# Kernel tuning notes

Measured on AMD Instinct MI355X. Metric: run time of the kernel, lower is better.

## Reference

```python
import jax, jax.numpy as jnp
import numpy as np

B, S, D = 4, 4096, 1024
DC = 1024  # d_chunk (defaults to d_model)
NUM_CLASSES = 4


def setup_inputs() -> dict:
    key = jax.random.key(0)
    ks = jax.random.split(key, 8)
    init = lambda k, shape: (jax.random.normal(k, shape, jnp.float32) * 0.02)
    return {
        "h": jax.random.normal(ks[0], (B, S, D), jnp.float32),
        "pseudo_labels": jax.random.randint(ks[1], (B, S), 0, NUM_CLASSES, jnp.int32),
        "Wl": init(ks[2], (D, NUM_CLASSES)), "bl": jnp.zeros((NUM_CLASSES,), jnp.float32),
        "Wq": init(ks[3], (D, DC)), "bq": jnp.zeros((DC,), jnp.float32),
        "Wk": init(ks[4], (D, DC)), "bk": jnp.zeros((DC,), jnp.float32),
        "Wv": init(ks[5], (D, D)), "bv": jnp.zeros((D,), jnp.float32),
        "Wo": init(ks[6], (D, D)), "bo": jnp.zeros((D,), jnp.float32),
    }


def _chunk_starts(labels):
    """BIOS chunking: label 0=B starts a chunk extended by following 1=I's;
    labels 1 (orphan I), 2=O, 3=S are singleton chunks. Returns bool [B,S]
    marking chunk starts. Parallel replacement for the torch while-loop."""
    def step(ext, lab):  # ext[b]: previous token can be extended by an I
        cont = (lab == 1) & ext          # this token continues prev chunk
        new_ext = (lab == 0) | cont      # B, or a continuing I, is extendable
        return new_ext, ~cont            # non-continuing token starts a chunk
    init = jnp.zeros(labels.shape[0], dtype=bool)
    _, starts_t = jax.lax.scan(step, init, labels.T)  # scan over seq axis
    return starts_t.T  # [B, S]


def reference(h, pseudo_labels, Wl, bl, Wq, bq, Wk, bk, Wv, bv, Wo, bo):
    b, s, d = h.shape
    dc = Wq.shape[1]

    logits = h @ Wl + bl                                  # [B,S,4]
    logp = jax.nn.log_softmax(logits, axis=-1)
    loss = -jnp.mean(jnp.take_along_axis(logp, pseudo_labels[..., None], axis=-1))

    pred = jnp.argmax(logits, axis=-1).astype(jnp.int32)  # [B,S]
    starts = _chunk_starts(pred)
    seg = jnp.cumsum(starts.astype(jnp.int32), axis=1) - 1  # segment id per token

    # Segment-mean pooling, padded to S possible chunks per batch element.
    seg_sum = jax.vmap(lambda x, ids: jax.ops.segment_sum(x, ids, num_segments=s))(h, seg)
    counts = jax.vmap(lambda ids: jax.ops.segment_sum(jnp.ones((s,), h.dtype), ids, num_segments=s))(seg)
    chunk_emb = seg_sum / jnp.maximum(counts, 1.0)[..., None]  # [B,S,D]
    valid = counts > 0                                         # [B,S]

    q = h @ Wq + bq              # [B,S,DC]
    k = chunk_emb @ Wk + bk      # [B,C,DC]
    v = chunk_emb @ Wv + bv      # [B,C,D]
    scale = jnp.asarray(1.0 / np.sqrt(dc), h.dtype)
    scores = jnp.einsum('bsd,bcd->bsc', q, k) * scale
    scores = jnp.where(valid[:, None, :], scores, jnp.asarray(-1e30, h.dtype))
    attn = jax.nn.softmax(scores, axis=-1)
    attended = jnp.einsum('bsc,bcd->bsd', attn, v)
    ch_out = attended @ Wo + bo
    return ch_out, loss
```

## Files before the change

kernel.cpp:

```cpp
#include <hip/hip_runtime.h>

typedef unsigned short u16;
typedef __attribute__((ext_vector_type(8))) short short8;
typedef __attribute__((ext_vector_type(8))) unsigned short ushort8;
typedef __attribute__((ext_vector_type(4))) unsigned short ushort4v;
typedef __attribute__((ext_vector_type(4))) float f32x4;

#define NB 4
#define SS 4096
#define DD 1024

__device__ __forceinline__ u16 f2bf(float x) {
  unsigned u = __builtin_bit_cast(unsigned, x);
  u = (u + 0x7FFFu + ((u >> 16) & 1u)) >> 16;
  return (u16)u;
}
__device__ __forceinline__ float bf2f(u16 b) {
  unsigned u = ((unsigned)b) << 16;
  return __builtin_bit_cast(float, u);
}
__device__ __forceinline__ void gload16(const void* g, void* l) {
  __builtin_amdgcn_global_load_lds((const __attribute__((address_space(1))) void*)g,
                                   (__attribute__((address_space(3))) void*)l, 16, 0, 0);
}
__device__ __forceinline__ int xcd_swz(int bid, int nwg) {
  const int x = bid & 7, idx = bid >> 3;
  const int q = nwg >> 3, r = nwg & 7;
  return (x < r ? x * (q + 1) : r * (q + 1) + (x - r) * q) + idx;
}

__global__ __launch_bounds__(256) void k_logits(
    const float* __restrict__ h, const int* __restrict__ lab,
    const float* __restrict__ Wl, const float* __restrict__ bl,
    u16* __restrict__ h16, int* __restrict__ pred, float* __restrict__ lossPart)
{
  const int t = threadIdx.x, w = t >> 6, lane = t & 63;
  const int tok = blockIdx.x * 4 + w;
  const float4* h4p = (const float4*)(h + (size_t)tok * DD);
  const float4* wl4 = (const float4*)Wl;
  float p0 = 0.f, p1 = 0.f, p2 = 0.f, p3 = 0.f;
#pragma unroll
  for (int i = 0; i < 4; ++i) {
    const int d = i * 256 + lane * 4;
    float4 hv = h4p[i * 64 + lane];
    ushort4v hb;
    hb[0] = f2bf(hv.x); hb[1] = f2bf(hv.y); hb[2] = f2bf(hv.z); hb[3] = f2bf(hv.w);
    *(ushort4v*)(h16 + (size_t)tok * DD + d) = hb;
    float4 w0 = wl4[d], w1 = wl4[d + 1], w2 = wl4[d + 2], w3 = wl4[d + 3];
    p0 += hv.x * w0.x + hv.y * w1.x + hv.z * w2.x + hv.w * w3.x;
    p1 += hv.x * w0.y + hv.y * w1.y + hv.z * w2.y + hv.w * w3.y;
    p2 += hv.x * w0.z + hv.y * w1.z + hv.z * w2.z + hv.w * w3.z;
    p3 += hv.x * w0.w + hv.y * w1.w + hv.z * w2.w + hv.w * w3.w;
  }
#pragma unroll
  for (int m = 32; m; m >>= 1) {
    p0 += __shfl_xor(p0, m); p1 += __shfl_xor(p1, m);
    p2 += __shfl_xor(p2, m); p3 += __shfl_xor(p3, m);
  }
  __shared__ float ls[4];
  if (lane == 0) {
    float l[4] = {p0 + bl[0], p1 + bl[1], p2 + bl[2], p3 + bl[3]};
    int bi = 0; float bv = l[0];
#pragma unroll
    for (int c = 1; c < 4; ++c) if (l[c] > bv) { bv = l[c]; bi = c; }
    pred[tok] = bi;
    float se = 0.f;
#pragma unroll
    for (int c = 0; c < 4; ++c) se += expf(l[c] - bv);
    float lse = bv + logf(se);
    ls[w] = lse - l[lab[tok]];
  }
  __syncthreads();
  if (t == 0) lossPart[blockIdx.x] = ls[0] + ls[1] + ls[2] + ls[3];
}

__global__ __launch_bounds__(256) void k_wconv(
    const float* __restrict__ W0, const float* __restrict__ W1,
    const float* __restrict__ W2, const float* __restrict__ W3,
    u16* __restrict__ Wt)
{
  const int gid = blockIdx.x * 256 + threadIdx.x;
  const int mat = gid >> 20;
  const int rem = gid & ((1 << 20) - 1);
  const int n = rem >> 10, k = rem & 1023;
  const float* W = (mat == 0) ? W0 : (mat == 1) ? W1 : (mat == 2) ? W2 : W3;
  Wt[((size_t)mat << 20) + (size_t)n * 1024 + k] = f2bf(W[(size_t)k * 1024 + n]);
}

__global__ __launch_bounds__(256) void k_scan(
    const int* __restrict__ pred, int* __restrict__ cstart, int* __restrict__ ccnt)
{
  const int b = blockIdx.x, t = threadIdx.x;
  const int4* p4 = (const int4*)(pred + (size_t)b * SS);
  int labv[16];
#pragma unroll
  for (int i = 0; i < 4; ++i) {
    int4 v = p4[t * 4 + i];
    labv[i * 4 + 0] = v.x; labv[i * 4 + 1] = v.y;
    labv[i * 4 + 2] = v.z; labv[i * 4 + 3] = v.w;
  }
  int A = 0, Bc = 1;
#pragma unroll
  for (int e = 0; e < 16; ++e) {
    int a = (labv[e] == 0), bb = (labv[e] == 1);
    A = a | (bb & A);
    Bc = bb & Bc;
  }
  __shared__ int sA[256], sB[256], sC[256];
  sA[t] = A; sB[t] = Bc;
  __syncthreads();
  for (int off = 1; off < 256; off <<= 1) {
    int pa = 0, pb = 1;
    if (t >= off) { pa = sA[t - off]; pb = sB[t - off]; }
    __syncthreads();
    A = A | (Bc & pa); Bc = Bc & pb;
    sA[t] = A; sB[t] = Bc;
    __syncthreads();
  }
  const int extIn = (t == 0) ? 0 : sA[t - 1];
  int ext = extIn, nst = 0;
#pragma unroll
  for (int e = 0; e < 16; ++e) {
    int cont = (labv[e] == 1) & ext;
    nst += !cont;
    ext = (labv[e] == 0) | cont;
  }
  sC[t] = nst;
  __syncthreads();
  int tot = nst;
  for (int off = 1; off < 256; off <<= 1) {
    int pc = 0;
    if (t >= off) pc = sC[t - off];
    __syncthreads();
    tot += pc;
    sC[t] = tot;
    __syncthreads();
  }
  const int base = tot - nst;
  const int total = sC[255];
  if (t == 0) { ccnt[b] = total; cstart[b * (SS + 1) + total] = SS; }
  ext = extIn; int id = base;
#pragma unroll
  for (int e = 0; e < 16; ++e) {
    int cont = (labv[e] == 1) & ext;
    if (!cont) cstart[b * (SS + 1) + id++] = t * 16 + e;
    ext = (labv[e] == 0) | cont;
  }
}

__global__ __launch_bounds__(256) void k_pool(
    const float* __restrict__ h, const int* __restrict__ cstart,
    const int* __restrict__ ccnt, u16* __restrict__ cemb)
{
  const int t = threadIdx.x, w = t >> 6, lane = t & 63;
  const int gw = blockIdx.x * 4 + w;
  const int b = gw >> 12, c = gw & (SS - 1);
  u16* out = cemb + (size_t)gw * DD + lane * 16;
  if (c >= ccnt[b]) {
    ushort8 z = {0, 0, 0, 0, 0, 0, 0, 0};
    *(ushort8*)out = z; *(ushort8*)(out + 8) = z;
    return;
  }
  const int s0 = cstart[b * (SS + 1) + c], s1 = cstart[b * (SS + 1) + c + 1];
  float acc[16] = {};
  for (int s = s0; s < s1; ++s) {
    const float4* hp = (const float4*)(h + ((size_t)b * SS + s) * DD + lane * 16);
#pragma unroll
    for (int ii = 0; ii < 4; ++ii) {
      float4 v = hp[ii];
      acc[ii * 4 + 0] += v.x; acc[ii * 4 + 1] += v.y;
      acc[ii * 4 + 2] += v.z; acc[ii * 4 + 3] += v.w;
    }
  }
  const float inv = 1.f / (float)(s1 - s0);
  ushort8 o0, o1;
#pragma unroll
  for (int e = 0; e < 8; ++e) { o0[e] = f2bf(acc[e] * inv); o1[e] = f2bf(acc[8 + e] * inv); }
  *(ushort8*)out = o0; *(ushort8*)(out + 8) = o1;
}

template <int OUTF32>
__global__ __launch_bounds__(512, 2) void gemm256(
    const u16* __restrict__ A0, const u16* __restrict__ A1,
    const u16* __restrict__ A2, const u16* __restrict__ A3,
    const u16* __restrict__ Bt, long strideB,
    void* __restrict__ C0, void* __restrict__ C1,
    void* __restrict__ C2, void* __restrict__ C3,
    const float* __restrict__ bias, float scale, int M, int N, int K)
{
  __shared__ u16 sA[2][256 * 64], sB[2][256 * 64];
  const int t = threadIdx.x, lane = t & 63, w = t >> 6;
  const int wr = w >> 2, wc = w & 3;
  const int z = blockIdx.z;
  const u16* A = (z == 0) ? A0 : (z == 1) ? A1 : (z == 2) ? A2 : A3;
  void* Cp    = (z == 0) ? C0 : (z == 1) ? C1 : (z == 2) ? C2 : C3;
  const u16* B = Bt + (size_t)z * strideB;
  const int bid = blockIdx.y * gridDim.x + blockIdx.x;
  const int swz = xcd_swz(bid, gridDim.x * gridDim.y);
  const int m0 = (swz / gridDim.x) * 256, n0 = (swz % gridDim.x) * 256;

  f32x4 acc[8][4];
#pragma unroll
  for (int i = 0; i < 8; ++i)
#pragma unroll
    for (int j = 0; j < 4; ++j) acc[i][j] = (f32x4){0.f, 0.f, 0.f, 0.f};

  const int trow = t >> 3;
  const int schunk = ((t & 7) ^ (trow & 7)) * 8;
  const u16* Ag = A + (size_t)(m0 + trow) * K + schunk;
  const u16* Bg = B + (size_t)(n0 + trow) * K + schunk;
  u16* lA = &sA[0][0] + t * 8;
  u16* lB = &sB[0][0] + t * 8;
  auto stage = [&](int c, int kt) {
#pragma unroll
    for (int g = 0; g < 4; ++g)
      gload16(Ag + (size_t)(g * 64) * K + kt, lA + c * 16384 + g * 4096);
#pragma unroll
    for (int g = 0; g < 4; ++g)
      gload16(Bg + (size_t)(g * 64) * K + kt, lB + c * 16384 + g * 4096);
  };

  const int lrow = lane & 15, hi = lane >> 4, sx = lrow & 7;
  auto compute = [&](int c) {
    const u16* bA = &sA[c][0];
    const u16* bB = &sB[c][0];
#pragma unroll
    for (int ks = 0; ks < 2; ++ks) {
      const int co = ((ks * 4 + hi) ^ sx) * 8;
      short8 af[8], bf[4];
#pragma unroll
      for (int m = 0; m < 8; ++m)
        af[m] = *(const short8*)(bA + (wr * 128 + m * 16 + lrow) * 64 + co);
#pragma unroll
      for (int n = 0; n < 4; ++n)
        bf[n] = *(const short8*)(bB + (wc * 64 + n * 16 + lrow) * 64 + co);
#pragma unroll
      for (int m = 0; m < 8; ++m)
#pragma unroll
        for (int n = 0; n < 4; ++n)
          acc[m][n] = __builtin_amdgcn_mfma_f32_16x16x32_bf16(af[m], bf[n], acc[m][n], 0, 0, 0);
    }
  };

  const int NT = K >> 6;
  stage(0, 0);
  if (NT > 1) { stage(1, 64); asm volatile("s_waitcnt vmcnt(8)" ::: "memory"); }
  else        { asm volatile("s_waitcnt vmcnt(0)" ::: "memory"); }
  __builtin_amdgcn_s_barrier();
  asm volatile("" ::: "memory");
  for (int i = 0; i < NT; ++i) {
    const int cur = i & 1;
    compute(cur);
    asm volatile("" ::: "memory");
    if (i + 2 < NT) {
      __builtin_amdgcn_s_barrier();
      asm volatile("" ::: "memory");
      stage(cur, (i + 2) * 64);
    }
    if (i + 1 < NT) {
      if (i + 2 < NT) asm volatile("s_waitcnt vmcnt(8)" ::: "memory");
      else            asm volatile("s_waitcnt vmcnt(0)" ::: "memory");
      __builtin_amdgcn_s_barrier();
      asm volatile("" ::: "memory");
    }
  }

  const int colb = n0 + wc * 64 + (lane & 15);
  const int rowb = m0 + wr * 128 + (lane >> 4) * 4;
#pragma unroll
  for (int n = 0; n < 4; ++n) {
    const int col = colb + n * 16;
    const float bv = bias ? bias[col] : 0.f;
#pragma unroll
    for (int m = 0; m < 8; ++m) {
#pragma unroll
      for (int qx = 0; qx < 4; ++qx) {
        const float v = acc[m][n][qx] * scale + bv;
        const size_t idx = (size_t)(rowb + m * 16 + qx) * N + col;
        if (OUTF32) ((float*)Cp)[idx] = v;
        else        ((u16*)Cp)[idx]  = f2bf(v);
      }
    }
  }
}

__global__ __launch_bounds__(256) void k_softmax(
    u16* __restrict__ s0, u16* __restrict__ s1,
    u16* __restrict__ s2, u16* __restrict__ s3, const int* __restrict__ ccnt)
{
  const int t = threadIdx.x, lane = t & 63, w = t >> 6;
  const int row = blockIdx.x, b = blockIdx.y;
  u16* sc = (b == 0) ? s0 : (b == 1) ? s1 : (b == 2) ? s2 : s3;
  const int Cb = ccnt[b];
  u16* p = sc + (size_t)row * SS + t * 16;
  ushort8 v0 = *(ushort8*)p, v1 = *(ushort8*)(p + 8);
  float x[16];
#pragma unroll
  for (int e = 0; e < 8; ++e) { x[e] = bf2f(v0[e]); x[8 + e] = bf2f(v1[e]); }
  const int cb0 = t * 16;
  float m = -1e30f;
#pragma unroll
  for (int e = 0; e < 16; ++e) if (cb0 + e < Cb) m = fmaxf(m, x[e]);
#pragma unroll
  for (int off = 32; off; off >>= 1) m = fmaxf(m, __shfl_xor(m, off));
  __shared__ float red[4], red2[4];
  if (lane == 0) red[w] = m;
  __syncthreads();
  m = fmaxf(fmaxf(red[0], red[1]), fmaxf(red[2], red[3]));
  float ssum = 0.f;
#pragma unroll
  for (int e = 0; e < 16; ++e) {
    float ev = (cb0 + e < Cb) ? __expf(x[e] - m) : 0.f;
    x[e] = ev; ssum += ev;
  }
#pragma unroll
  for (int off = 32; off; off >>= 1) ssum += __shfl_xor(ssum, off);
  if (lane == 0) red2[w] = ssum;
  __syncthreads();
  ssum = red2[0] + red2[1] + red2[2] + red2[3];
  const float inv = 1.f / ssum;
#pragma unroll
  for (int e = 0; e < 8; ++e) { v0[e] = f2bf(x[e] * inv); v1[e] = f2bf(x[8 + e] * inv); }
  *(ushort8*)p = v0; *(ushort8*)(p + 8) = v1;
}

__global__ __launch_bounds__(256) void k_transpose(
    const u16* __restrict__ v, u16* __restrict__ vt)
{
  __shared__ u16 ts[64][80];
  const int t = threadIdx.x;
  const int d0 = blockIdx.x * 64, c0 = blockIdx.y * 64, b = blockIdx.z;
#pragma unroll
  for (int p = 0; p < 2; ++p) {
    const int idx = p * 256 + t, r = idx >> 3, cc = idx & 7;
    ushort8 val = *(const ushort8*)(v + ((size_t)b * SS + c0 + r) * DD + d0 + cc * 8);
    *(ushort8*)&ts[r][cc * 8] = val;
  }
  __syncthreads();
#pragma unroll
  for (int p = 0; p < 2; ++p) {
    const int idx = p * 256 + t, r = idx >> 3, cc = idx & 7;
    ushort8 o;
#pragma unroll
    for (int e = 0; e < 8; ++e) o[e] = ts[cc * 8 + e][r];
    *(ushort8*)(vt + ((size_t)b * DD + d0 + r) * SS + c0 + cc * 8) = o;
  }
}

__global__ __launch_bounds__(256) void k_lossfin(
    const float* __restrict__ part, float* __restrict__ out)
{
  const int t = threadIdx.x, lane = t & 63, w = t >> 6;
  float s = 0.f;
  for (int i = t; i < 4096; i += 256) s += part[i];
#pragma unroll
  for (int off = 32; off; off >>= 1) s += __shfl_xor(s, off);
  __shared__ float r[4];
  if (lane == 0) r[w] = s;
  __syncthreads();
  if (t == 0) out[0] = (r[0] + r[1] + r[2] + r[3]) * (1.f / (NB * SS));
}

extern "C" void kernel_launch(void* const* d_in, const int* in_sizes, int n_in,
                              void* d_out, int out_size, void* d_ws, size_t ws_size,
                              hipStream_t stream) {
  const float* h  = (const float*)d_in[0];
  const int* plab = (const int*)d_in[1];
  const float* Wl = (const float*)d_in[2];
  const float* bl = (const float*)d_in[3];
  const float* Wq = (const float*)d_in[4];
  const float* bq = (const float*)d_in[5];
  const float* Wk = (const float*)d_in[6];
  const float* bk = (const float*)d_in[7];
  const float* Wv = (const float*)d_in[8];
  const float* bv = (const float*)d_in[9];
  const float* Wo = (const float*)d_in[10];
  const float* bo = (const float*)d_in[11];
  float* out = (float*)d_out;

  char* ws = (char*)d_ws;
  const size_t SZ = (size_t)NB * SS * DD * 2;
  const size_t SD = (size_t)SS * DD;
  u16* h16      = (u16*)(ws + 0 * SZ);
  u16* cemb     = (u16*)(ws + 1 * SZ);
  u16* q        = (u16*)(ws + 2 * SZ);
  u16* kk       = (u16*)(ws + 3 * SZ);
  u16* vv       = (u16*)(ws + 4 * SZ);
  u16* vt       = (u16*)(ws + 5 * SZ);
  u16* Wt       = (u16*)(ws + 6 * SZ);
  char* ws2     = ws + 6 * SZ + (size_t)4 * 1024 * 1024 * 2;
  int* pred     = (int*)ws2;
  int* cstart   = (int*)(ws2 + 65536);
  int* ccnt     = (int*)(ws2 + 65536 + 4 * (SS + 1) * 4);
  float* lossPart = (float*)(ws2 + 65536 + 4 * (SS + 1) * 4 + 64);
  u16* s0 = (u16*)d_out;
  u16* s1 = (u16*)d_out + (size_t)SS * SS;
  u16* s2 = h16;
  u16* s3 = cemb;
  u16* att = vv;

  k_logits<<<dim3(NB * SS / 4), 256, 0, stream>>>(h, plab, Wl, bl, h16, pred, lossPart);
  k_wconv<<<dim3(4 * 1024 * 1024 / 256), 256, 0, stream>>>(Wq, Wk, Wv, Wo, Wt);
  k_scan<<<dim3(NB), 256, 0, stream>>>(pred, cstart, ccnt);
  k_pool<<<dim3(NB * SS / 4), 256, 0, stream>>>(h, cstart, ccnt, cemb);

  gemm256<0><<<dim3(DD / 256, NB * SS / 256, 1), 512, 0, stream>>>(
      h16, h16, h16, h16, Wt, 0, q, q, q, q, bq, 1.f, NB * SS, DD, DD);
  gemm256<0><<<dim3(DD / 256, NB * SS / 256, 1), 512, 0, stream>>>(
      cemb, cemb, cemb, cemb, Wt + (1 << 20), 0, kk, kk, kk, kk, bk, 1.f, NB * SS, DD, DD);
  gemm256<0><<<dim3(DD / 256, NB * SS / 256, 1), 512, 0, stream>>>(
      cemb, cemb, cemb, cemb, Wt + 2 * (1 << 20), 0, vv, vv, vv, vv, bv, 1.f, NB * SS, DD, DD);
  k_transpose<<<dim3(DD / 64, SS / 64, NB), 256, 0, stream>>>(vv, vt);

  const float scl = 1.f / 32.f;
  gemm256<0><<<dim3(SS / 256, SS / 256, NB), 512, 0, stream>>>(
      q, q + SD, q + 2 * SD, q + 3 * SD, kk, (long)SD,
      s0, s1, s2, s3, nullptr, scl, SS, SS, DD);
  k_softmax<<<dim3(SS, NB), 256, 0, stream>>>(s0, s1, s2, s3, ccnt);
  gemm256<0><<<dim3(DD / 256, SS / 256, NB), 512, 0, stream>>>(
      s0, s1, s2, s3, vt, (long)SD,
      att, att + SD, att + 2 * SD, att + 3 * SD, nullptr, 1.f, SS, DD, SS);
  gemm256<1><<<dim3(DD / 256, NB * SS / 256, 1), 512, 0, stream>>>(
      att, att, att, att, Wt + 3 * (1 << 20), 0, out, out, out, out, bo, 1.f, NB * SS, DD, DD);
  k_lossfin<<<dim3(1), 256, 0, stream>>>(lossPart, out + (size_t)NB * SS * DD);
}
```

Baseline: 640.1 us.

## Restructure GEMM main loop into four-phase interleaved load/MFMA schedule with LDS-staged epilogue

Rewrites the 256x256 bf16 GEMM main loop so each K-tile is split into four quadrant phases. Each phase issues part of the next tiles' global-to-LDS loads, then runs a block of MFMAs under raised wave priority, with barriers and sched_barriers fencing the stages. The bf16 output path now stages results through LDS and writes 16-byte coalesced rows instead of scattered 2-byte stores. The aim is better overlap of memory traffic with MFMA work and cheaper stores. The cost is many more barriers per iteration and a changed column mapping of warps to tiles.

```diff
diff --git a/kernel.cpp b/kernel.cpp
--- a/kernel.cpp
+++ b/kernel.cpp
@@ -9,6 +9,7 @@
 #define NB 4
 #define SS 4096
 #define DD 1024
+#define CFENCE asm volatile("" ::: "memory")
 
 __device__ __forceinline__ u16 f2bf(float x) {
   unsigned u = __builtin_bit_cast(unsigned, x);
@@ -188,7 +189,9 @@
     void* __restrict__ C2, void* __restrict__ C3,
     const float* __restrict__ bias, float scale, int M, int N, int K)
 {
-  __shared__ u16 sA[2][256 * 64], sB[2][256 * 64];
+  __shared__ u16 lds[65536];
+  u16* ldsA = lds;
+  u16* ldsB = lds + 32768;
   const int t = threadIdx.x, lane = t & 63, w = t >> 6;
   const int wr = w >> 2, wc = w & 3;
   const int z = blockIdx.z;
@@ -206,82 +209,144 @@
     for (int j = 0; j < 4; ++j) acc[i][j] = (f32x4){0.f, 0.f, 0.f, 0.f};
 
   const int trow = t >> 3;
-  const int schunk = ((t & 7) ^ (trow & 7)) * 8;
-  const u16* Ag = A + (size_t)(m0 + trow) * K + schunk;
-  const u16* Bg = B + (size_t)(n0 + trow) * K + schunk;
-  u16* lA = &sA[0][0] + t * 8;
-  u16* lB = &sB[0][0] + t * 8;
-  auto stage = [&](int c, int kt) {
-#pragma unroll
-    for (int g = 0; g < 4; ++g)
-      gload16(Ag + (size_t)(g * 64) * K + kt, lA + c * 16384 + g * 4096);
-#pragma unroll
-    for (int g = 0; g < 4; ++g)
-      gload16(Bg + (size_t)(g * 64) * K + kt, lB + c * 16384 + g * 4096);
-  };
-
-  const int lrow = lane & 15, hi = lane >> 4, sx = lrow & 7;
-  auto compute = [&](int c) {
-    const u16* bA = &sA[c][0];
-    const u16* bB = &sB[c][0];
-#pragma unroll
-    for (int ks = 0; ks < 2; ++ks) {
-      const int co = ((ks * 4 + hi) ^ sx) * 8;
-      short8 af[8], bf[4];
+  const u16* Ag = A + (size_t)(m0 + trow) * K + ((t & 7) ^ (trow & 7)) * 8;
+  const u16* Bg = B + (size_t)(n0 + trow) * K + ((t & 7) ^ (trow & 7)) * 8;
+  u16* dA = ldsA + t * 8;
+  u16* dB = ldsB + t * 8;
+
+#define STG_A0(BUF, KT) { gload16(Ag + (size_t)(KT),            dA + (BUF) * 16384 + 0 * 4096); \
+                          gload16(Ag + (size_t)128 * K + (KT),  dA + (BUF) * 16384 + 2 * 4096); }
+#define STG_A1(BUF, KT) { gload16(Ag + (size_t)64 * K + (KT),   dA + (BUF) * 16384 + 1 * 4096); \
+                          gload16(Ag + (size_t)192 * K + (KT),  dA + (BUF) * 16384 + 3 * 4096); }
+#define STG_B0(BUF, KT) { gload16(Bg + (size_t)(KT),            dB + (BUF) * 16384 + 0 * 4096); \
+                          gload16(Bg + (size_t)64 * K + (KT),   dB + (BUF) * 16384 + 1 * 4096); }
+#define STG_B1(BUF, KT) { gload16(Bg + (size_t)128 * K + (KT),  dB + (BUF) * 16384 + 2 * 4096); \
+                          gload16(Bg + (size_t)192 * K + (KT),  dB + (BUF) * 16384 + 3 * 4096); }
+#define MFMA16(MH, NH, BF) \
+  { _Pragma("unroll") for (int ks = 0; ks < 2; ++ks) \
+    _Pragma("unroll") for (int mi = 0; mi < 4; ++mi) \
+      _Pragma("unroll") for (int ni = 0; ni < 2; ++ni) \
+        acc[(MH) * 4 + mi][(NH) * 2 + ni] = __builtin_amdgcn_mfma_f32_16x16x32_bf16( \
+            af[mi][ks], BF[ni][ks], acc[(MH) * 4 + mi][(NH) * 2 + ni], 0, 0, 0); }
+
+  const int lrow = lane & 15, hi = lane >> 4;
+  const int co0 = (hi ^ (lrow & 7)) * 8;
+  const int co1 = ((4 + hi) ^ (lrow & 7)) * 8;
+
+  const int NT = K >> 6;
+  STG_A0(0, 0); STG_B0(0, 0); STG_B1(0, 0); STG_A1(0, 0);
+  if (NT > 1) { STG_A0(1, 64); STG_B0(1, 64); STG_B1(1, 64); }
+  if (NT > 1) asm volatile("s_waitcnt vmcnt(6)" ::: "memory");
+  else        asm volatile("s_waitcnt vmcnt(0)" ::: "memory");
+  __builtin_amdgcn_s_barrier();
+  CFENCE;
+
+  for (int j = 0; j < NT; ++j) {
+    const int cur = j & 1;
+    const u16* bA = ldsA + cur * 16384;
+    const u16* bB = ldsB + cur * 16384;
+    const int kt1 = (j + 1) << 6, kt2 = (j + 2) << 6;
+    short8 af[4][2], b0[2][2], b1[2][2];
+#pragma unroll
+    for (int mi = 0; mi < 4; ++mi) {
+      af[mi][0] = *(const short8*)(bA + (wr * 128 + mi * 16 + lrow) * 64 + co0);
+      af[mi][1] = *(const short8*)(bA + (wr * 128 + mi * 16 + lrow) * 64 + co1);
+    }
+#pragma unroll
+    for (int ni = 0; ni < 2; ++ni) {
+      b0[ni][0] = *(const short8*)(bB + (wc * 32 + ni * 16 + lrow) * 64 + co0);
+      b0[ni][1] = *(const short8*)(bB + (wc * 32 + ni * 16 + lrow) * 64 + co1);
+    }
+    if (j + 1 < NT) STG_A1(cur ^ 1, kt1);
+    CFENCE;
+    __builtin_amdgcn_s_barrier();
+    __builtin_amdgcn_s_setprio(1);
+    MFMA16(0, 0, b0);
+    __builtin_amdgcn_s_setprio(0);
+    __builtin_amdgcn_sched_barrier(0);
+    __builtin_amdgcn_s_barrier();
+    CFENCE;
+#pragma unroll
+    for (int ni = 0; ni < 2; ++ni) {
+      b1[ni][0] = *(const short8*)(bB + (128 + wc * 32 + ni * 16 + lrow) * 64 + co0);
+      b1[ni][1] = *(const short8*)(bB + (128 + wc * 32 + ni * 16 + lrow) * 64 + co1);
+    }
+    if (j + 2 < NT) STG_A0(cur, kt2);
+    CFENCE;
+    __builtin_amdgcn_s_barrier();
+    __builtin_amdgcn_s_setprio(1);
+    MFMA16(0, 1, b1);
+    __builtin_amdgcn_s_setprio(0);
+    __builtin_amdgcn_sched_barrier(0);
+    __builtin_amdgcn_s_barrier();
+    CFENCE;
+#pragma unroll
+    for (int mi = 0; mi < 4; ++mi) {
+      af[mi][0] = *(const short8*)(bA + (wr * 128 + 64 + mi * 16 + lrow) * 64 + co0);
+      af[mi][1] = *(const short8*)(bA + (wr * 128 + 64 + mi * 16 + lrow) * 64 + co1);
+    }
+    if (j + 2 < NT) STG_B0(cur, kt2);
+    CFENCE;
+    __builtin_amdgcn_s_barrier();
+    __builtin_amdgcn_s_setprio(1);
+    MFMA16(1, 0, b0);
+    __builtin_amdgcn_s_setprio(0);
+    __builtin_amdgcn_sched_barrier(0);
+    __builtin_amdgcn_s_barrier();
+    CFENCE;
+    if (j + 2 < NT) STG_B1(cur, kt2);
+    CFENCE;
+    __builtin_amdgcn_s_barrier();
+    __builtin_amdgcn_s_setprio(1);
+    MFMA16(1, 1, b1);
+    __builtin_amdgcn_s_setprio(0);
+    if (j < NT - 2)       asm volatile("s_waitcnt vmcnt(6)" ::: "memory");
+    else if (j == NT - 2) asm volatile("s_waitcnt vmcnt(0)" ::: "memory");
+    __builtin_amdgcn_sched_barrier(0);
+    __builtin_amdgcn_s_barrier();
+    CFENCE;
+  }
+
+  if (OUTF32) {
+    const int rowb = m0 + wr * 128 + (lane >> 4) * 4;
+#pragma unroll
+    for (int n = 0; n < 4; ++n) {
+      const int col = n0 + (n >> 1) * 128 + wc * 32 + (n & 1) * 16 + (lane & 15);
+      const float bv = bias ? bias[col] : 0.f;
 #pragma unroll
       for (int m = 0; m < 8; ++m)
-        af[m] = *(const short8*)(bA + (wr * 128 + m * 16 + lrow) * 64 + co);
-#pragma unroll
-      for (int n = 0; n < 4; ++n)
-        bf[n] = *(const short8*)(bB + (wc * 64 + n * 16 + lrow) * 64 + co);
+#pragma unroll
+        for (int q = 0; q < 4; ++q)
+          ((float*)Cp)[(size_t)(rowb + m * 16 + q) * N + col] = acc[m][n][q] * scale + bv;
+    }
+  } else {
+    u16* cls = lds;
+    const int rowl = wr * 128 + (lane >> 4) * 4;
+#pragma unroll
+    for (int n = 0; n < 4; ++n) {
+      const int coll = (n >> 1) * 128 + wc * 32 + (n & 1) * 16 + (lane & 15);
+      const float bv = bias ? bias[n0 + coll] : 0.f;
 #pragma unroll
       for (int m = 0; m < 8; ++m)
 #pragma unroll
-        for (int n = 0; n < 4; ++n)
-          acc[m][n] = __builtin_amdgcn_mfma_f32_16x16x32_bf16(af[m], bf[n], acc[m][n], 0, 0, 0);
-    }
-  };
-
-  const int NT = K >> 6;
-  stage(0, 0);
-  if (NT > 1) { stage(1, 64); asm volatile("s_waitcnt vmcnt(8)" ::: "memory"); }
-  else        { asm volatile("s_waitcnt vmcnt(0)" ::: "memory"); }
-  __builtin_amdgcn_s_barrier();
-  asm volatile("" ::: "memory");
-  for (int i = 0; i < NT; ++i) {
-    const int cur = i & 1;
-    compute(cur);
-    asm volatile("" ::: "memory");
-    if (i + 2 < NT) {
-      __builtin_amdgcn_s_barrier();
-      asm volatile("" ::: "memory");
-      stage(cur, (i + 2) * 64);
-    }
-    if (i + 1 < NT) {
-      if (i + 2 < NT) asm volatile("s_waitcnt vmcnt(8)" ::: "memory");
-      else            asm volatile("s_waitcnt vmcnt(0)" ::: "memory");
-      __builtin_amdgcn_s_barrier();
-      asm volatile("" ::: "memory");
-    }
-  }
-
-  const int colb = n0 + wc * 64 + (lane & 15);
-  const int rowb = m0 + wr * 128 + (lane >> 4) * 4;
-#pragma unroll
-  for (int n = 0; n < 4; ++n) {
-    const int col = colb + n * 16;
-    const float bv = bias ? bias[col] : 0.f;
-#pragma unroll
-    for (int m = 0; m < 8; ++m) {
-#pragma unroll
-      for (int qx = 0; qx < 4; ++qx) {
-        const float v = acc[m][n][qx] * scale + bv;
-        const size_t idx = (size_t)(rowb + m * 16 + qx) * N + col;
-        if (OUTF32) ((float*)Cp)[idx] = v;
-        else        ((u16*)Cp)[idx]  = f2bf(v);
-      }
-    }
-  }
+        for (int q = 0; q < 4; ++q)
+          cls[(rowl + m * 16 + q) * 256 + coll] = f2bf(acc[m][n][q] * scale + bv);
+    }
+    __syncthreads();
+    u16* Cu = (u16*)Cp;
+#pragma unroll
+    for (int ps = 0; ps < 16; ++ps) {
+      const int f = ps * 512 + t;
+      const int row = f >> 5, col8 = (f & 31) * 8;
+      *(ushort8*)(Cu + (size_t)(m0 + row) * N + n0 + col8) =
+          *(const ushort8*)(cls + row * 256 + col8);
+    }
+  }
+#undef STG_A0
+#undef STG_A1
+#undef STG_B0
+#undef STG_B1
+#undef MFMA16
 }
 
 __global__ __launch_bounds__(256) void k_softmax(
```

Measured after the change: 535.2 us. -16.4%, faster.
